# Kernel tuning notes

Hardware: AMD Instinct MI355X
Metric: run time of the kernel (lower is better)

Reference implementation:

```python
import jax, jax.numpy as jnp
import numpy as np

B, N, CIN, H, UNITS = 8, 2048, 256, 256, 256


def setup_inputs() -> dict:
    key = jax.random.key(0)
    ks = jax.random.split(key, 7)
    s = 1.0 / np.sqrt(CIN)
    return {
        "x": jax.random.normal(ks[0], (B, N, CIN), dtype=jnp.float32),
        "Wq": jax.random.normal(ks[1], (CIN, H), dtype=jnp.float32) * s,
        "bq": jax.random.normal(ks[2], (H,), dtype=jnp.float32) * 0.01,
        "Wk": jax.random.normal(ks[3], (CIN, H), dtype=jnp.float32) * s,
        "bk": jax.random.normal(ks[4], (H,), dtype=jnp.float32) * 0.01,
        "Wm": jax.random.normal(ks[5], (H, UNITS), dtype=jnp.float32) * (1.0 / np.sqrt(H)),
        "bm": jax.random.normal(ks[6], (UNITS,), dtype=jnp.float32) * 0.01,
    }


def reference(x, Wq, bq, Wk, bk, Wm, bm):
    # Dense projections with fused relu (as in the Keras module)
    q = jax.nn.relu(x @ Wq + bq)          # (B,N,H)
    k = jax.nn.relu(x @ Wk + bk)          # (B,N,H)
    v = q                                 # NOTE: source uses fc_query for value (fc_value unused)
    # Unscaled key @ query^T, softmax over last axis
    kq = jax.nn.softmax(jnp.einsum('bnh,bmh->bnm', k, q), axis=-1)  # (B,N,N)
    # value^T @ kq, then Permute((2,1)): att[b,m,h] = sum_n v[b,n,h] * kq[b,n,m]
    att = jnp.einsum('bnh,bnm->bmh', v, kq)                          # (B,N,H)
    return jax.nn.relu(att @ Wm + bm)                                # (B,N,UNITS)
```

## Files before the change

kernel.cpp:

```cpp
#include <hip/hip_runtime.h>
#include <hip/hip_bf16.h>
#include <math.h>

#define BB   8
#define NN   2048
#define CC   256
#define MTOT (BB * NN)

typedef __bf16 bf16_t;
typedef bf16_t    bf16x8 __attribute__((ext_vector_type(8)));
typedef _Float16  halfx8 __attribute__((ext_vector_type(8)));
typedef float     floatx4 __attribute__((ext_vector_type(4)));

#define LOG2E 1.44269504088896f

__device__ __forceinline__ void gl_lds16(const bf16_t* g, bf16_t* l) {
    __builtin_amdgcn_global_load_lds(
        (const __attribute__((address_space(1))) unsigned int*)g,
        (__attribute__((address_space(3))) unsigned int*)l, 16, 0, 0);
}

template<int OMODE, bool BIASRELU, bool DO_STATS>
__global__ __launch_bounds__(256, 3)
void gemm_nt(const bf16_t* __restrict__ A, const bf16_t* __restrict__ B,
             void* __restrict__ C, const float* __restrict__ bias,
             int lda, int ldb, int ldc,
             long strideA, long strideB, long strideC,
             float* __restrict__ pm, float* __restrict__ pl)
{
    const int b = blockIdx.z;
    A += (long)b * strideA;
    B += (long)b * strideB;
    const int m0 = blockIdx.y * 128;
    const int n0 = blockIdx.x * 128;

    __shared__ bf16_t As[128 * 32];
    __shared__ bf16_t Bs[128 * 32];
    __shared__ float  smx[4][4][16];
    __shared__ float  ssm[4][4][16];

    const int tid  = threadIdx.x;
    const int wid  = tid >> 6, lane = tid & 63;
    const int wm   = (wid >> 1) * 64, wn = (wid & 1) * 64;
    const int fr   = lane & 15;
    const int kb   = (lane >> 4) * 8;

    floatx4 acc[4][4] = {};

    for (int k0 = 0; k0 < 256; k0 += 32) {
#pragma unroll
        for (int r = 0; r < 2; ++r) {
            const int lin = tid + r * 256;
            const int rw  = lin >> 2, kc = lin & 3;
            gl_lds16(A + (long)(m0 + rw) * lda + k0 + kc * 8, As + lin * 8);
            gl_lds16(B + (long)(n0 + rw) * ldb + k0 + kc * 8, Bs + lin * 8);
        }
        __syncthreads();
        bf16x8 af[4], bf[4];
#pragma unroll
        for (int f = 0; f < 4; ++f) {
            af[f] = *(const bf16x8*)(As + (wm + f * 16 + fr) * 32 + kb);
            bf[f] = *(const bf16x8*)(Bs + (wn + f * 16 + fr) * 32 + kb);
        }
#pragma unroll
        for (int f = 0; f < 4; ++f)
#pragma unroll
            for (int g = 0; g < 4; ++g)
                acc[f][g] = __builtin_amdgcn_mfma_f32_16x16x32_bf16(af[f], bf[g], acc[f][g], 0, 0, 0);
        __syncthreads();
    }

    const int rbase = (lane >> 4) * 4;
#pragma unroll
    for (int g = 0; g < 4; ++g) {
        const int n = n0 + wn + g * 16 + fr;
        const float bv = BIASRELU ? bias[n] : 0.0f;
#pragma unroll
        for (int f = 0; f < 4; ++f) {
#pragma unroll
            for (int r = 0; r < 4; ++r) {
                const int m = m0 + wm + f * 16 + rbase + r;
                float v = acc[f][g][r] + bv;
                if (BIASRELU) v = v > 0.0f ? v : 0.0f;
                if (OMODE == 0)
                    ((float*)C)[(long)b * strideC + (long)m * ldc + n] = v;
                else if (OMODE == 1)
                    ((bf16_t*)C)[(long)b * strideC + (long)m * ldc + n] = (bf16_t)v;
                else
                    ((_Float16*)C)[(long)b * strideC + (long)m * ldc + n] = (_Float16)v;
            }
        }
    }

    if (DO_STATS) {
        float lmax[4], lsum[4];
#pragma unroll
        for (int g = 0; g < 4; ++g) {
            float m = -1e30f;
#pragma unroll
            for (int f = 0; f < 4; ++f)
#pragma unroll
                for (int r = 0; r < 4; ++r) m = fmaxf(m, acc[f][g][r]);
            m = fmaxf(m, __shfl_xor(m, 16));
            m = fmaxf(m, __shfl_xor(m, 32));
            float s = 0.0f;
#pragma unroll
            for (int f = 0; f < 4; ++f)
#pragma unroll
                for (int r = 0; r < 4; ++r) s += __expf(acc[f][g][r] - m);
            s += __shfl_xor(s, 16);
            s += __shfl_xor(s, 32);
            lmax[g] = m; lsum[g] = s;
        }
        if (lane < 16) {
#pragma unroll
            for (int g = 0; g < 4; ++g) {
                smx[wid][g][lane] = lmax[g];
                ssm[wid][g][lane] = lsum[g];
            }
        }
        __syncthreads();
        if (tid < 128) {
            const int pair = tid >> 6;
            const int idx  = tid & 63;
            const int g = idx >> 4, f2 = idx & 15;
            const float m0v = smx[pair][g][f2], m1v = smx[pair + 2][g][f2];
            const float M = fmaxf(m0v, m1v);
            const float L = ssm[pair][g][f2] * __expf(m0v - M) +
                            ssm[pair + 2][g][f2] * __expf(m1v - M);
            const int n = n0 + pair * 64 + g * 16 + f2;
            const long o = ((long)b * 16 + blockIdx.y) * NN + n;
            pm[o] = M;
            pl[o] = L;
        }
    }
}

__global__ __launch_bounds__(256)
void stats_combine(const float* __restrict__ pm, const float* __restrict__ pl,
                   float* __restrict__ c2)
{
    const int i = blockIdx.x * 256 + threadIdx.x;
    const int b = i >> 11, n = i & 2047;
    float M = -1e30f, L = 0.0f;
#pragma unroll
    for (int t = 0; t < 16; ++t) {
        const long o = ((long)b * 16 + t) * NN + n;
        const float m = pm[o], l = pl[o];
        const float nm = fmaxf(M, m);
        L = L * __expf(M - nm) + l * __expf(m - nm);
        M = nm;
    }
    c2[i] = (M + logf(L)) * LOG2E;
}

#define APAD 68
__global__ __launch_bounds__(256, 4)
void att_out(const _Float16* __restrict__ St, const bf16_t* __restrict__ qmT,
             const float* __restrict__ c2, const float* __restrict__ bm,
             float* __restrict__ out)
{
    const int b  = blockIdx.z;
    const int m0 = blockIdx.x * 32;
    const int u0 = blockIdx.y * 128;
    const _Float16* S  = St  + (long)b * NN * NN;
    const bf16_t*   Q  = qmT + (long)b * 256 * NN;
    const float*    C2 = c2  + b * NN;
    float*          O  = out + (long)b * NN * 256;

    __shared__ bf16_t As[32 * APAD];
    __shared__ bf16_t Bs[128 * 64];

    const int tid  = threadIdx.x;
    const int wid  = tid >> 6, lane = tid & 63;
    const int wm2  = (wid >> 1) * 16;
    const int wu   = (wid & 1) * 64;
    const int fr   = lane & 15;
    const int u16  = lane >> 4;
    const int kb   = u16 * 8;
    const int fsw  = fr & 7;
    const int arow = tid >> 3;
    const int aseg = tid & 7;

    const _Float16* Srow = S + (long)(m0 + arow) * NN + aseg * 8;

    floatx4 acc[4] = {};

    for (int n0 = 0; n0 < NN; n0 += 64) {
#pragma unroll
        for (int r = 0; r < 4; ++r) {
            const int lin = tid + r * 256;
            const int rw  = lin >> 3, kc = lin & 7;
            const int kcs = kc ^ (rw & 7);
            gl_lds16(Q + (long)(u0 + rw) * NN + n0 + kcs * 8, Bs + lin * 8);
        }
        const halfx8 hv = *(const halfx8*)(Srow + n0);
        const float4 ca = *(const float4*)(C2 + n0 + aseg * 8);
        const float4 cb = *(const float4*)(C2 + n0 + aseg * 8 + 4);
        bf16x8 p;
        p[0] = (bf16_t)exp2f(fmaf((float)hv[0], LOG2E, -ca.x));
        p[1] = (bf16_t)exp2f(fmaf((float)hv[1], LOG2E, -ca.y));
        p[2] = (bf16_t)exp2f(fmaf((float)hv[2], LOG2E, -ca.z));
        p[3] = (bf16_t)exp2f(fmaf((float)hv[3], LOG2E, -ca.w));
        p[4] = (bf16_t)exp2f(fmaf((float)hv[4], LOG2E, -cb.x));
        p[5] = (bf16_t)exp2f(fmaf((float)hv[5], LOG2E, -cb.y));
        p[6] = (bf16_t)exp2f(fmaf((float)hv[6], LOG2E, -cb.z));
        p[7] = (bf16_t)exp2f(fmaf((float)hv[7], LOG2E, -cb.w));
        *(bf16x8*)(As + arow * APAD + aseg * 8) = p;
        __syncthreads();

        bf16x8 af[2], bg[4][2];
#pragma unroll
        for (int j = 0; j < 2; ++j)
            af[j] = *(const bf16x8*)(As + (wm2 + fr) * APAD + j * 32 + kb);
#pragma unroll
        for (int g = 0; g < 4; ++g)
#pragma unroll
            for (int j = 0; j < 2; ++j) {
                const int chunk = (j * 4 + u16) ^ fsw;
                bg[g][j] = *(const bf16x8*)(Bs + (wu + g * 16 + fr) * 64 + chunk * 8);
            }
#pragma unroll
        for (int j = 0; j < 2; ++j)
#pragma unroll
            for (int g = 0; g < 4; ++g)
                acc[g] = __builtin_amdgcn_mfma_f32_16x16x32_bf16(af[j], bg[g][j], acc[g], 0, 0, 0);
        __syncthreads();
    }

    const int rbase = u16 * 4;
#pragma unroll
    for (int g = 0; g < 4; ++g) {
        const int u = u0 + wu + g * 16 + fr;
        const float bvv = bm[u];
#pragma unroll
        for (int r = 0; r < 4; ++r) {
            const int m = m0 + wm2 + rbase + r;
            const float v = acc[g][r] + bvv;
            O[(long)m * 256 + u] = v > 0.0f ? v : 0.0f;
        }
    }
}

__global__ __launch_bounds__(256)
void cvt_bf16(const float* __restrict__ x, bf16_t* __restrict__ y)
{
    const long i = ((long)blockIdx.x * 256 + threadIdx.x) * 8;
    const float4 a = *(const float4*)(x + i);
    const float4 b = *(const float4*)(x + i + 4);
    bf16x8 o;
    o[0] = (bf16_t)a.x; o[1] = (bf16_t)a.y; o[2] = (bf16_t)a.z; o[3] = (bf16_t)a.w;
    o[4] = (bf16_t)b.x; o[5] = (bf16_t)b.y; o[6] = (bf16_t)b.z; o[7] = (bf16_t)b.w;
    *(bf16x8*)(y + i) = o;
}

__global__ __launch_bounds__(256)
void prep_w(const float* __restrict__ Wq, const float* __restrict__ Wk,
            const float* __restrict__ Wm, const float* __restrict__ bq,
            const float* __restrict__ bk, bf16_t* __restrict__ WqkT,
            bf16_t* __restrict__ WmT, float* __restrict__ bqk)
{
    const int z = blockIdx.z;
    const float* W = (z == 0) ? Wq : (z == 1) ? Wk : Wm;
    bf16_t* Wt = (z == 0) ? WqkT : (z == 1) ? (WqkT + 256 * 256) : WmT;
    __shared__ float t[32][33];
    const int n0 = blockIdx.x * 32, k0 = blockIdx.y * 32;
    const int tx = threadIdx.x & 31, ty = threadIdx.x >> 5;
    for (int i = ty; i < 32; i += 8) t[i][tx] = W[(k0 + i) * 256 + n0 + tx];
    __syncthreads();
    for (int i = ty; i < 32; i += 8) Wt[(n0 + i) * 256 + k0 + tx] = (bf16_t)t[tx][i];
    if (z == 0 && blockIdx.x == 0 && blockIdx.y == 0) {
        bqk[threadIdx.x]       = bq[threadIdx.x];
        bqk[256 + threadIdx.x] = bk[threadIdx.x];
    }
}

extern "C" void kernel_launch(void* const* d_in, const int* in_sizes, int n_in,
                              void* d_out, int out_size, void* d_ws, size_t ws_size,
                              hipStream_t stream)
{
    (void)in_sizes; (void)n_in; (void)out_size; (void)ws_size;
    const float* x  = (const float*)d_in[0];
    const float* Wq = (const float*)d_in[1];
    const float* bq = (const float*)d_in[2];
    const float* Wk = (const float*)d_in[3];
    const float* bk = (const float*)d_in[4];
    const float* Wm = (const float*)d_in[5];
    const float* bm = (const float*)d_in[6];
    float* out = (float*)d_out;

    char* w = (char*)d_ws;
    _Float16* St   = (_Float16*)w;                  w += (size_t)BB * NN * NN * 2;
    bf16_t* x_bf   = (bf16_t*)w;                    w += (size_t)MTOT * 256 * 2;
    bf16_t* qk     = (bf16_t*)w;                    w += (size_t)MTOT * 512 * 2;
    bf16_t* qmT    = (bf16_t*)w;                    w += (size_t)MTOT * 256 * 2;
    bf16_t* WqkT   = (bf16_t*)w;                    w += 512 * 256 * 2;
    bf16_t* WmT    = (bf16_t*)w;                    w += 256 * 256 * 2;
    float*  bqk    = (float*)w;                     w += 512 * 4;
    float*  pm     = (float*)w;                     w += (size_t)BB * 16 * NN * 4;
    float*  pl     = (float*)w;                     w += (size_t)BB * 16 * NN * 4;
    float*  c2b    = (float*)w;

    cvt_bf16<<<dim3(MTOT * 256 / (256 * 8)), 256, 0, stream>>>(x, x_bf);
    prep_w<<<dim3(8, 8, 3), 256, 0, stream>>>(Wq, Wk, Wm, bq, bk, WqkT, WmT, bqk);

    gemm_nt<1, true, false><<<dim3(4, 128, 1), 256, 0, stream>>>(
        x_bf, WqkT, qk, bqk, 256, 256, 512, 0, 0, 0, nullptr, nullptr);

    gemm_nt<1, false, false><<<dim3(16, 2, BB), 256, 0, stream>>>(
        WmT, qk, qmT, nullptr, 256, 512, NN,
        0, (long)NN * 512, (long)256 * NN, nullptr, nullptr);

    gemm_nt<2, false, true><<<dim3(16, 16, BB), 256, 0, stream>>>(
        qk, qk + 256, St, nullptr, 512, 512, NN,
        (long)NN * 512, (long)NN * 512, (long)NN * NN, pm, pl);

    stats_combine<<<dim3(MTOT / 256), 256, 0, stream>>>(pm, pl, c2b);

    att_out<<<dim3(64, 2, BB), 256, 0, stream>>>(St, qmT, c2b, bm, out);
}
```

Baseline: 179.1 us.

## Retile att_out to 128-row tiles with direct register P and double-buffered Q

Reshapes att_out so each block covers 128 query rows by 64 output units, with each wave owning 32 rows. The fp16 scores are loaded straight into registers in MFMA operand layout, exponentiated there, and fed to the MFMAs without staging through LDS. The Q operand tiles are double-buffered in LDS and the next scores are prefetched a step ahead. This is meant to cut redundant Q reloads and one LDS round trip and barrier per step, at the cost of more registers and lower occupancy (launch bound 2).

```diff
diff --git a/kernel.cpp b/kernel.cpp
--- a/kernel.cpp
+++ b/kernel.cpp
@@ -154,91 +154,120 @@
     c2[i] = (M + logf(L)) * LOG2E;
 }
 
-#define APAD 68
-__global__ __launch_bounds__(256, 4)
+__global__ __launch_bounds__(256, 2)
 void att_out(const _Float16* __restrict__ St, const bf16_t* __restrict__ qmT,
              const float* __restrict__ c2, const float* __restrict__ bm,
              float* __restrict__ out)
 {
     const int b  = blockIdx.z;
-    const int m0 = blockIdx.x * 32;
-    const int u0 = blockIdx.y * 128;
+    const int m0 = blockIdx.x * 128;
+    const int u0 = blockIdx.y * 64;
     const _Float16* S  = St  + (long)b * NN * NN;
     const bf16_t*   Q  = qmT + (long)b * 256 * NN;
     const float*    C2 = c2  + b * NN;
     float*          O  = out + (long)b * NN * 256;
 
-    __shared__ bf16_t As[32 * APAD];
-    __shared__ bf16_t Bs[128 * 64];
+    __shared__ bf16_t Bs0[64 * 64];
+    __shared__ bf16_t Bs1[64 * 64];
 
     const int tid  = threadIdx.x;
     const int wid  = tid >> 6, lane = tid & 63;
-    const int wm2  = (wid >> 1) * 16;
-    const int wu   = (wid & 1) * 64;
+    const int wm2  = wid * 32;
     const int fr   = lane & 15;
     const int u16  = lane >> 4;
-    const int kb   = u16 * 8;
     const int fsw  = fr & 7;
-    const int arow = tid >> 3;
-    const int aseg = tid & 7;
-
-    const _Float16* Srow = S + (long)(m0 + arow) * NN + aseg * 8;
-
-    floatx4 acc[4] = {};
-
-    for (int n0 = 0; n0 < NN; n0 += 64) {
-#pragma unroll
-        for (int r = 0; r < 4; ++r) {
-            const int lin = tid + r * 256;
-            const int rw  = lin >> 3, kc = lin & 7;
-            const int kcs = kc ^ (rw & 7);
-            gl_lds16(Q + (long)(u0 + rw) * NN + n0 + kcs * 8, Bs + lin * 8);
-        }
-        const halfx8 hv = *(const halfx8*)(Srow + n0);
-        const float4 ca = *(const float4*)(C2 + n0 + aseg * 8);
-        const float4 cb = *(const float4*)(C2 + n0 + aseg * 8 + 4);
-        bf16x8 p;
-        p[0] = (bf16_t)exp2f(fmaf((float)hv[0], LOG2E, -ca.x));
-        p[1] = (bf16_t)exp2f(fmaf((float)hv[1], LOG2E, -ca.y));
-        p[2] = (bf16_t)exp2f(fmaf((float)hv[2], LOG2E, -ca.z));
-        p[3] = (bf16_t)exp2f(fmaf((float)hv[3], LOG2E, -ca.w));
-        p[4] = (bf16_t)exp2f(fmaf((float)hv[4], LOG2E, -cb.x));
-        p[5] = (bf16_t)exp2f(fmaf((float)hv[5], LOG2E, -cb.y));
-        p[6] = (bf16_t)exp2f(fmaf((float)hv[6], LOG2E, -cb.z));
-        p[7] = (bf16_t)exp2f(fmaf((float)hv[7], LOG2E, -cb.w));
-        *(bf16x8*)(As + arow * APAD + aseg * 8) = p;
-        __syncthreads();
-
-        bf16x8 af[2], bg[4][2];
-#pragma unroll
-        for (int j = 0; j < 2; ++j)
-            af[j] = *(const bf16x8*)(As + (wm2 + fr) * APAD + j * 32 + kb);
+
+    const _Float16* Sr0 = S + (long)(m0 + wm2 + fr) * NN + u16 * 8;
+    const _Float16* Sr1 = Sr0 + 16 * NN;
+
+    const int rw0 = tid >> 3, kc0 = tid & 7;
+
+    floatx4 acc[2][4] = {};
+
+    gl_lds16(Q + (long)(u0 + rw0) * NN + (kc0 ^ (rw0 & 7)) * 8, Bs0 + tid * 8);
+    gl_lds16(Q + (long)(u0 + 32 + rw0) * NN + (kc0 ^ (rw0 & 7)) * 8,
+             Bs0 + (256 + tid) * 8);
+    halfx8 ap[4];
+    ap[0] = *(const halfx8*)(Sr0);
+    ap[1] = *(const halfx8*)(Sr0 + 32);
+    ap[2] = *(const halfx8*)(Sr1);
+    ap[3] = *(const halfx8*)(Sr1 + 32);
+    __syncthreads();
+
+    for (int i = 0; i < 32; ++i) {
+        const int n0 = i * 64;
+        const bf16_t* Brd = (i & 1) ? Bs1 : Bs0;
+        bf16_t*       Bwr = (i & 1) ? Bs0 : Bs1;
+
+        halfx8 ac[4];
+#pragma unroll
+        for (int t = 0; t < 4; ++t) ac[t] = ap[t];
+
+        if (i < 31) {
+            const int n1 = n0 + 64;
+            gl_lds16(Q + (long)(u0 + rw0) * NN + n1 + (kc0 ^ (rw0 & 7)) * 8,
+                     Bwr + tid * 8);
+            gl_lds16(Q + (long)(u0 + 32 + rw0) * NN + n1 + (kc0 ^ (rw0 & 7)) * 8,
+                     Bwr + (256 + tid) * 8);
+            ap[0] = *(const halfx8*)(Sr0 + n1);
+            ap[1] = *(const halfx8*)(Sr0 + n1 + 32);
+            ap[2] = *(const halfx8*)(Sr1 + n1);
+            ap[3] = *(const halfx8*)(Sr1 + n1 + 32);
+        }
+
+        bf16x8 p[4];
+#pragma unroll
+        for (int j = 0; j < 2; ++j) {
+            const float4 ca = *(const float4*)(C2 + n0 + j * 32 + u16 * 8);
+            const float4 cb = *(const float4*)(C2 + n0 + j * 32 + u16 * 8 + 4);
+#pragma unroll
+            for (int f = 0; f < 2; ++f) {
+                const halfx8 h = ac[f * 2 + j];
+                bf16x8 pp;
+                pp[0] = (bf16_t)exp2f(fmaf((float)h[0], LOG2E, -ca.x));
+                pp[1] = (bf16_t)exp2f(fmaf((float)h[1], LOG2E, -ca.y));
+                pp[2] = (bf16_t)exp2f(fmaf((float)h[2], LOG2E, -ca.z));
+                pp[3] = (bf16_t)exp2f(fmaf((float)h[3], LOG2E, -ca.w));
+                pp[4] = (bf16_t)exp2f(fmaf((float)h[4], LOG2E, -cb.x));
+                pp[5] = (bf16_t)exp2f(fmaf((float)h[5], LOG2E, -cb.y));
+                pp[6] = (bf16_t)exp2f(fmaf((float)h[6], LOG2E, -cb.z));
+                pp[7] = (bf16_t)exp2f(fmaf((float)h[7], LOG2E, -cb.w));
+                p[f * 2 + j] = pp;
+            }
+        }
+
+        bf16x8 bg[4][2];
 #pragma unroll
         for (int g = 0; g < 4; ++g)
 #pragma unroll
             for (int j = 0; j < 2; ++j) {
                 const int chunk = (j * 4 + u16) ^ fsw;
-                bg[g][j] = *(const bf16x8*)(Bs + (wu + g * 16 + fr) * 64 + chunk * 8);
+                bg[g][j] = *(const bf16x8*)(Brd + (g * 16 + fr) * 64 + chunk * 8);
             }
 #pragma unroll
         for (int j = 0; j < 2; ++j)
 #pragma unroll
-            for (int g = 0; g < 4; ++g)
-                acc[g] = __builtin_amdgcn_mfma_f32_16x16x32_bf16(af[j], bg[g][j], acc[g], 0, 0, 0);
+            for (int f = 0; f < 2; ++f)
+#pragma unroll
+                for (int g = 0; g < 4; ++g)
+                    acc[f][g] = __builtin_amdgcn_mfma_f32_16x16x32_bf16(
+                        p[f * 2 + j], bg[g][j], acc[f][g], 0, 0, 0);
         __syncthreads();
     }
 
     const int rbase = u16 * 4;
 #pragma unroll
     for (int g = 0; g < 4; ++g) {
-        const int u = u0 + wu + g * 16 + fr;
+        const int u = u0 + g * 16 + fr;
         const float bvv = bm[u];
 #pragma unroll
-        for (int r = 0; r < 4; ++r) {
-            const int m = m0 + wm2 + rbase + r;
-            const float v = acc[g][r] + bvv;
-            O[(long)m * 256 + u] = v > 0.0f ? v : 0.0f;
-        }
+        for (int f = 0; f < 2; ++f)
+#pragma unroll
+            for (int r = 0; r < 4; ++r) {
+                const int m = m0 + wm2 + f * 16 + rbase + r;
+                const float v = acc[f][g][r] + bvv;
+                O[(long)m * 256 + u] = v > 0.0f ? v : 0.0f;
+            }
     }
 }
 
@@ -317,5 +346,5 @@
 
     stats_combine<<<dim3(MTOT / 256), 256, 0, stream>>>(pm, pl, c2b);
 
-    att_out<<<dim3(64, 2, BB), 256, 0, stream>>>(St, qmT, c2b, bm, out);
-}
+    att_out<<<dim3(16, 4, BB), 256, 0, stream>>>(St, qmT, c2b, bm, out);
+}
```

Measured after the change: 195.0 us. 8.9% more time.
